# Kernel tuning notes

Measured on AMD Instinct MI355X. Metric: run time of the kernel, lower is better.

Reference implementation:

```python
import jax, jax.numpy as jnp
import numpy as np

VEC_DIM = 128   # D (also the per-head dim in this module)
HEADS = 8
PATCH = 4
WIN = 7
N_BATCH = 4
H_IMG = 448
W_IMG = 448


def _relative_index():
    # Swin-style relative position index, computed statically (matches torch code
    # which uses torch.meshgrid with default 'ij' indexing).
    coords = np.stack(np.meshgrid(np.arange(WIN), np.arange(WIN), indexing='ij'))  # [2,W,W]
    flat = coords.reshape(2, -1)                      # [2, W*W]
    rel = flat[:, :, None] - flat[:, None, :]         # [2, p, p]
    rel = rel.transpose(1, 2, 0).astype(np.int64)     # [p, p, 2]
    rel[:, :, 0] += WIN - 1
    rel[:, :, 1] += WIN - 1
    rel[:, :, 1] *= 2 * WIN - 1
    return rel.sum(-1)                                # [p, p], values in [0, (2W-1)^2)

REL_IDX = jnp.asarray(_relative_index())


def setup_inputs() -> dict:
    key = jax.random.key(0)
    ks = jax.random.split(key, 8)
    P = (H_IMG // PATCH) * (W_IMG // PATCH)  # 12544
    D, H = VEC_DIM, HEADS
    s = 0.02
    return {
        'x': jax.random.normal(ks[0], (N_BATCH, D, P), jnp.float32),
        'Wq': jax.random.normal(ks[1], (H * D, D), jnp.float32) * s,
        'bq': jnp.zeros((H * D,), jnp.float32),
        'Wk': jax.random.normal(ks[2], (H * D, D), jnp.float32) * s,
        'bk': jnp.zeros((H * D,), jnp.float32),
        'Wv': jax.random.normal(ks[3], (H * D, D), jnp.float32) * s,
        'bv': jnp.zeros((H * D,), jnp.float32),
        'Wo': jax.random.normal(ks[4], (D, H * D), jnp.float32) * s,
        'bo': jnp.zeros((D,), jnp.float32),
        'pos_code': jax.random.normal(ks[5], ((2 * WIN - 1) ** 2, H), jnp.float32) * s,
        'h': H_IMG,
        'w': W_IMG,
    }


def reference(x, Wq, bq, Wk, bk, Wv, bv, Wo, bo, pos_code, h, w):
    N, D, P = x.shape
    H = HEADS
    ch, cw = h // PATCH, w // PATCH
    nh, nw = ch // WIN, cw // WIN            # windows per axis
    p = WIN * WIN                            # tokens per window

    def emb(W, b):
        # pointwise Conv1d: [N,D,P] -> [N,H*D,P] -> [N,H,D,P]
        return (jnp.einsum('od,ndp->nop', W, x) + b[None, :, None]).reshape(N, H, D, P)

    def partition(e):
        # [N,H,D,P] -> [N,H,win_num,D,p]
        e = e.reshape(N, H, D, nh, WIN, nw, WIN)
        return e.transpose(0, 1, 3, 5, 2, 4, 6).reshape(N, H, nh * nw, D, p)

    q = partition(emb(Wq, bq))
    k = partition(emb(Wk, bk))
    v = partition(emb(Wv, bv))

    # attn[n,h,w,i,j] = sum_d k[n,h,w,d,i] * q[n,h,w,d,j], scaled
    attn = jnp.einsum('nhwdi,nhwdj->nhwij', k, q) / (D ** 0.5)
    bias = pos_code[REL_IDX].transpose(2, 0, 1)          # [H, p, p]
    attn = attn + bias[None, :, None, :, :]
    weights = jax.nn.softmax(attn, axis=3)               # softmax over key index i

    # out[n,h,w,d,j] = sum_i v[n,h,w,d,i] * weights[n,h,w,i,j]
    out = jnp.einsum('nhwdi,nhwij->nhwdj', v, weights)

    # window merge: [N,H,win_num,D,p] -> [N,H*D,P]
    out = out.reshape(N, H, nh, nw, D, WIN, WIN)
    out = out.transpose(0, 1, 4, 2, 5, 3, 6).reshape(N, H * D, P)

    return jnp.einsum('od,ndp->nop', Wo, out) + bo[None, :, None]
```

## Files before the change

kernel.cpp:

```cpp
#include <hip/hip_runtime.h>
#include <hip/hip_bf16.h>

typedef unsigned short u16;
typedef unsigned int u32;
typedef __attribute__((ext_vector_type(8))) short bf16x8;
typedef __attribute__((ext_vector_type(4))) float f32x4;
typedef __attribute__((ext_vector_type(2))) unsigned int u32x2;

#define NBATCH 4
#define DDIM   128
#define NHEAD  8
#define PTOT   12544
#define CWID   112
#define NTOK   49
#define PSTR   68
#define SCALE  0.08838834764831845f

#define BUFSZ   14464
#undef BUFSZ
#define BUFSZ   16384
#define OFF_US  8192
#define OFF_PL  32768
#define OFF_PCF 36100
#define OFF_MF  38804
#define OFF_CS  40852
#define LDS_TOT 41876

#undef OFF_MF
#undef OFF_CS
#undef LDS_TOT
#define OFF_CS  38804
#define LDS_TOT 39828

__device__ __forceinline__ float bf2f(u16 u) {
    union { u32 i; float f; } x; x.i = ((u32)u) << 16; return x.f;
}
__device__ __forceinline__ u16 f2bf(float f) {
    union { float f; u32 u; } v; v.f = f;
    return (u16)((v.u + 0x7fffu + ((v.u >> 16) & 1u)) >> 16);
}
__device__ __forceinline__ u32 pk2(float a, float b) {
    union { __hip_bfloat162 h; u32 u; } c;
    float2 t; t.x = a; t.y = b;
    c.h = __float22bfloat162_rn(t);
    return c.u;
}
__device__ __forceinline__ int swz128(int row, int col) {
    return row * 128 + ((((col >> 3) ^ (row & 15)) & 15) << 3) + (col & 7);
}

#define WS_WC   131072
#define WS_F32  262144

__global__ void __launch_bounds__(256) prep(
    const float* __restrict__ Wq, const float* __restrict__ Wk,
    const float* __restrict__ Wv, const float* __restrict__ Wo,
    const float* __restrict__ bq, const float* __restrict__ bk,
    const float* __restrict__ bv, u16* __restrict__ ws)
{
    __shared__ u16 lm[32768];
    const int tid = threadIdx.x;
    const int b = blockIdx.x;
    const bool isG = (b >= 8);
    const int h = b & 7;
    float* fb = (float*)(ws + WS_F32);

    if (!isG) {
        for (int idx = tid; idx < 16384; idx += 256) {
            const int dd = idx >> 7, dh = idx & 127;
            lm[swz128(dd, dh)] = f2bf(Wo[dd * 1024 + h * 128 + dh]);
        }
        for (int idx = tid; idx < 16384; idx += 256) {
            const int dh = idx >> 7, d = idx & 127;
            lm[16384 + swz128(d, dh)] = f2bf(Wv[(h * 128 + dh) * 128 + d]);
        }
        if (tid < 128) {
            float s = 0.f;
            for (int dh = 0; dh < 128; ++dh)
                s += Wo[tid * 1024 + h * 128 + dh] * bv[h * 128 + dh];
            fb[h * 128 + tid] = s;
        }
    } else {
        for (int idx = tid; idx < 16384; idx += 256) {
            const int dh = idx >> 7, d = idx & 127;
            lm[swz128(d, dh)] = f2bf(Wk[(h * 128 + dh) * 128 + d]);
        }
        for (int idx = tid; idx < 16384; idx += 256) {
            const int dh = idx >> 7, dp = idx & 127;
            lm[16384 + swz128(dp, dh)] = f2bf(Wq[(h * 128 + dh) * 128 + dp]);
        }
        if (tid < 128) {
            float r = 0.f, m = 0.f;
            for (int dh = 0; dh < 128; ++dh) {
                r += bk[h * 128 + dh] * Wq[(h * 128 + dh) * 128 + tid];
                m += Wk[(h * 128 + dh) * 128 + tid] * bq[h * 128 + dh];
            }
            fb[1024 + h * 128 + tid] = r * SCALE;
            fb[2048 + h * 128 + tid] = m * SCALE;
        }
        if (tid == 0) {
            float s = 0.f;
            for (int dh = 0; dh < 128; ++dh) s += bk[h * 128 + dh] * bq[h * 128 + dh];
            fb[3072 + h] = s * SCALE;
        }
    }
    __syncthreads();

    const int w = tid >> 6, lane = tid & 63, quad = lane >> 4, lid = lane & 15;
    const f32x4 z4 = {0.f, 0.f, 0.f, 0.f};
    u16* dst = ws + (isG ? 0 : WS_WC) + h * 16384;
    const float gs = isG ? SCALE : 1.0f;
    #pragma unroll
    for (int mtl = 0; mtl < 2; ++mtl) {
        const int mt = 2 * w + mtl;
        bf16x8 A[4];
        #pragma unroll
        for (int kt = 0; kt < 4; ++kt)
            A[kt] = *(const bf16x8*)(lm + swz128(mt * 16 + lid, kt * 32 + quad * 8));
        #pragma unroll
        for (int nt = 0; nt < 8; ++nt) {
            f32x4 acc = z4;
            #pragma unroll
            for (int kt = 0; kt < 4; ++kt) {
                bf16x8 B = *(const bf16x8*)(lm + 16384 + swz128(nt * 16 + lid, kt * 32 + quad * 8));
                acc = __builtin_amdgcn_mfma_f32_16x16x32_bf16(A[kt], B, acc, 0, 0, 0);
            }
            #pragma unroll
            for (int r = 0; r < 4; ++r) {
                const int row = mt * 16 + quad * 4 + r, col = nt * 16 + lid;
                if (isG) dst[col * 128 + row] = f2bf(acc[r] * gs);
                else     dst[row * 128 + col] = f2bf(acc[r]);
            }
        }
    }
}

__global__ void __launch_bounds__(256, 2)
winattn(const float* __restrict__ xg, const u16* __restrict__ ws,
        const float* __restrict__ bo, const float* __restrict__ posf,
        float* __restrict__ out)
{
    __shared__ __align__(16) u16 sm[LDS_TOT];
    u16* xw  = sm;
    u16* pl  = sm + OFF_PL;
    float* pcf = (float*)(sm + OFF_PCF);
    float* cs  = (float*)(sm + OFF_CS);

    const int tid  = threadIdx.x;
    const int w    = tid >> 6;
    const int lane = tid & 63;
    const int quad = lane >> 4;
    const int lid  = lane & 15;
    const int bx   = blockIdx.x;
    const int n    = bx >> 8;
    const int win  = bx & 255;
    const int pbase = (win >> 4) * 7 * CWID + (win & 15) * 7;

    const bf16x8 zf = {0,0,0,0,0,0,0,0};
    const f32x4  z4 = {0.f,0.f,0.f,0.f};

    const u16* Gt  = ws;
    const u16* Wcw = ws + WS_WC;
    const float* fb  = (const float*)(ws + WS_F32);
    const float* bcv = fb;
    const float* rP  = fb + 1024;
    const float* MP  = fb + 2048;
    const float* sP  = fb + 3072;

    for (int i = tid; i < 169 * NHEAD; i += 256) pcf[i] = posf[i];
    const float* xn = xg + n * DDIM * PTOT;
    for (int idx = tid; idx < DDIM * NTOK; idx += 256) {
        int d = idx / NTOK;
        int t = idx - d * NTOK;
        int a = t / 7, b = t - a * 7;
        xw[swz128(t, d)] = f2bf(xn[d * PTOT + pbase + a * CWID + b]);
    }
    __syncthreads();

    bf16x8 xfrag[4][4];
    #pragma unroll
    for (int mt = 0; mt < 4; ++mt)
        #pragma unroll
        for (int kt = 0; kt < 4; ++kt)
            xfrag[mt][kt] = (mt * 16 + lid < NTOK)
                ? *(const bf16x8*)(xw + swz128(mt * 16 + lid, kt * 32 + quad * 8)) : zf;
    const int j = 16 * w + lid;
    bf16x8 xq[4];
    #pragma unroll
    for (int kt = 0; kt < 4; ++kt)
        xq[kt] = (j < NTOK)
            ? *(const bf16x8*)(xw + swz128(j, kt * 32 + quad * 8)) : zf;

    for (int hh = w; hh < NHEAD; hh += 4) {
        const float sh = sP[hh];
        #pragma unroll
        for (int mt = 0; mt < 4; ++mt) {
            float c = 0.f;
            #pragma unroll
            for (int kt = 0; kt < 4; ++kt)
                #pragma unroll
                for (int jj = 0; jj < 8; ++jj)
                    c += bf2f((u16)xfrag[mt][kt][jj]) * MP[hh * 128 + kt * 32 + quad * 8 + jj];
            c += __shfl_xor(c, 16);
            c += __shfl_xor(c, 32);
            if (quad == 0) cs[hh * 64 + mt * 16 + lid] = c + sh;
        }
    }
    __syncthreads();

    f32x4 outacc[8];
    #pragma unroll
    for (int nt = 0; nt < 8; ++nt) outacc[nt] = z4;

    const int jc = j < NTOK ? j : NTOK - 1;

    for (int h = 0; h < NHEAD; ++h) {
        u16* tsb = sm + (h & 1) * BUFSZ;
        u16* usb = tsb + OFF_US;

        #pragma unroll
        for (int mtl = 0; mtl < 2; ++mtl) {
            const int mt = 2 * w + mtl;
            bf16x8 A[4];
            #pragma unroll
            for (int kt = 0; kt < 4; ++kt)
                A[kt] = *(const bf16x8*)(Gt + h * 16384 + (mt * 16 + lid) * 128 + kt * 32 + quad * 8);
            const f32x4 rb = *(const f32x4*)(rP + h * 128 + mt * 16 + quad * 4);
            const int dpb = mt * 16 + quad * 4;
            #pragma unroll
            for (int nt = 0; nt < 4; ++nt) {
                f32x4 acc = z4;
                #pragma unroll
                for (int kt = 0; kt < 4; ++kt)
                    acc = __builtin_amdgcn_mfma_f32_16x16x32_bf16(A[kt], xfrag[nt][kt], acc, 0, 0, 0);
                const int i = nt * 16 + lid;
                u32x2 pkv;
                pkv.x = pk2(acc[0] + rb[0], acc[1] + rb[1]);
                pkv.y = pk2(acc[2] + rb[2], acc[3] + rb[3]);
                *(u32x2*)(tsb + i * 128 + ((((dpb >> 3) ^ (i & 15)) & 15) << 3) + (dpb & 7)) = pkv;
            }
        }
        #pragma unroll
        for (int ntl = 0; ntl < 2; ++ntl) {
            const int nt = 2 * w + ntl;
            bf16x8 B[4];
            #pragma unroll
            for (int kt = 0; kt < 4; ++kt)
                B[kt] = *(const bf16x8*)(Wcw + h * 16384 + (nt * 16 + lid) * 128 + kt * 32 + quad * 8);
            const int dd = nt * 16 + lid;
            const float bb = bcv[h * 128 + dd];
            #pragma unroll
            for (int mt = 0; mt < 4; ++mt) {
                f32x4 acc = z4;
                #pragma unroll
                for (int kt = 0; kt < 4; ++kt)
                    acc = __builtin_amdgcn_mfma_f32_16x16x32_bf16(xfrag[mt][kt], B[kt], acc, 0, 0, 0);
                const int ib = mt * 16 + quad * 4;
                u32x2 pkv;
                pkv.x = pk2(acc[0] + bb, acc[1] + bb);
                pkv.y = pk2(acc[2] + bb, acc[3] + bb);
                *(u32x2*)(usb + dd * 64 + ((((ib >> 3) ^ (dd & 7)) & 7) << 3) + (ib & 7)) = pkv;
            }
        }
        __syncthreads();

        f32x4 S[4];
        #pragma unroll
        for (int mt = 0; mt < 4; ++mt) {
            S[mt] = z4;
            #pragma unroll
            for (int kt = 0; kt < 4; ++kt) {
                bf16x8 A = *(const bf16x8*)(tsb + (mt * 16 + lid) * 128 + ((((kt * 4 + quad) ^ lid) & 15) << 3));
                S[mt] = __builtin_amdgcn_mfma_f32_16x16x32_bf16(A, xq[kt], S[mt], 0, 0, 0);
            }
        }
        const int aj = jc / 7, bj = jc - aj * 7;
        float sv[4][4];
        float mx = -3.0e38f;
        #pragma unroll
        for (int mt = 0; mt < 4; ++mt)
            #pragma unroll
            for (int r = 0; r < 4; ++r) {
                const int ii = mt * 16 + quad * 4 + r;
                float vvv;
                if (ii < NTOK) {
                    const int ai = ii / 7, bi = ii - ai * 7;
                    const int rel = (ai - aj + 6) + 13 * (bi - bj + 6);
                    vvv = S[mt][r] + cs[h * 64 + ii] + pcf[rel * NHEAD + h];
                } else {
                    vvv = -3.0e38f;
                }
                sv[mt][r] = vvv;
                mx = fmaxf(mx, vvv);
            }
        mx = fmaxf(mx, __shfl_xor(mx, 16));
        mx = fmaxf(mx, __shfl_xor(mx, 32));
        float ssum = 0.f;
        #pragma unroll
        for (int mt = 0; mt < 4; ++mt)
            #pragma unroll
            for (int r = 0; r < 4; ++r) {
                const float e = __expf(sv[mt][r] - mx);
                sv[mt][r] = e;
                ssum += e;
            }
        ssum += __shfl_xor(ssum, 16);
        ssum += __shfl_xor(ssum, 32);
        const float inv = 1.0f / ssum;
        if (j < NTOK) {
            #pragma unroll
            for (int mt = 0; mt < 4; ++mt) {
                u32x2 pkv;
                pkv.x = pk2(sv[mt][0] * inv, sv[mt][1] * inv);
                pkv.y = pk2(sv[mt][2] * inv, sv[mt][3] * inv);
                *(u32x2*)(pl + j * PSTR + mt * 16 + quad * 4) = pkv;
            }
        }
        __threadfence_block();

        #pragma unroll
        for (int kt = 0; kt < 2; ++kt) {
            union { bf16x8 v; u32 u[4]; } Af;
            #pragma unroll
            for (int q2 = 0; q2 < 4; ++q2)
                Af.u[q2] = *(const u32*)(pl + jc * PSTR + kt * 32 + quad * 8 + 2 * q2);
            #pragma unroll
            for (int nt = 0; nt < 8; ++nt) {
                const int dd = nt * 16 + lid;
                bf16x8 Bu = *(const bf16x8*)(usb + dd * 64 + ((((kt * 4 + quad) ^ (dd & 7)) & 7) << 3));
                outacc[nt] = __builtin_amdgcn_mfma_f32_16x16x32_bf16(Af.v, Bu, outacc[nt], 0, 0, 0);
            }
        }
    }

    float* outp = out + n * DDIM * PTOT;
    #pragma unroll
    for (int nt = 0; nt < 8; ++nt) {
        const int dd = nt * 16 + lid;
        const float bov = bo[dd];
        #pragma unroll
        for (int r = 0; r < 4; ++r) {
            const int jj = 16 * w + quad * 4 + r;
            if (jj < NTOK) {
                const int a = jj / 7, b = jj - a * 7;
                outp[dd * PTOT + pbase + a * CWID + b] = outacc[nt][r] + bov;
            }
        }
    }
}

extern "C" void kernel_launch(void* const* d_in, const int* in_sizes, int n_in,
                              void* d_out, int out_size, void* d_ws, size_t ws_size,
                              hipStream_t stream) {
    (void)in_sizes; (void)n_in; (void)ws_size; (void)out_size;
    prep<<<16, 256, 0, stream>>>((const float*)d_in[1], (const float*)d_in[3],
                                 (const float*)d_in[5], (const float*)d_in[7],
                                 (const float*)d_in[2], (const float*)d_in[4],
                                 (const float*)d_in[6], (u16*)d_ws);
    winattn<<<NBATCH * 256, 256, 0, stream>>>(
        (const float*)d_in[0], (const u16*)d_ws,
        (const float*)d_in[8], (const float*)d_in[9], (float*)d_out);
}
```

Before: 236.6 us.

## Shrink LDS to single buffer, raise occupancy, and split prep across more blocks

The per-head T/U buffers are no longer double-buffered, and the positional-bias table is stored as bf16 in LDS. Together these cut shared memory roughly in half, so launch bounds rise to allow 4 blocks per CU. A __syncthreads at the end of each head iteration replaces the double-buffer hazard protection, and T stores are skipped for padding rows. The prep kernel is split into 128 blocks, each computing 16 output rows, to use more CUs; the trade-off is an extra barrier per head, possible register spills under the tighter bound, and slightly reduced bias precision.

```diff
diff --git a/kernel.cpp b/kernel.cpp
--- a/kernel.cpp
+++ b/kernel.cpp
@@ -16,21 +16,11 @@
 #define PSTR   68
 #define SCALE  0.08838834764831845f
 
-#define BUFSZ   14464
-#undef BUFSZ
-#define BUFSZ   16384
-#define OFF_US  8192
-#define OFF_PL  32768
-#define OFF_PCF 36100
-#define OFF_MF  38804
-#define OFF_CS  40852
-#define LDS_TOT 41876
-
-#undef OFF_MF
-#undef OFF_CS
-#undef LDS_TOT
-#define OFF_CS  38804
-#define LDS_TOT 39828
+#define OFF_US  6272
+#define OFF_PL  14464
+#define OFF_PCF 17796
+#define OFF_CS  19148
+#define LDS_TOT 20172
 
 __device__ __forceinline__ float bf2f(u16 u) {
     union { u32 i; float f; } x; x.i = ((u32)u) << 16; return x.f;
@@ -58,38 +48,41 @@
     const float* __restrict__ bq, const float* __restrict__ bk,
     const float* __restrict__ bv, u16* __restrict__ ws)
 {
-    __shared__ u16 lm[32768];
+    __shared__ u16 lm[18432];
     const int tid = threadIdx.x;
-    const int b = blockIdx.x;
+    const int bb  = blockIdx.x;
+    const int b   = bb >> 3;
+    const int sub = bb & 7;
     const bool isG = (b >= 8);
     const int h = b & 7;
+    const int r0 = sub * 16;
     float* fb = (float*)(ws + WS_F32);
 
     if (!isG) {
-        for (int idx = tid; idx < 16384; idx += 256) {
-            const int dd = idx >> 7, dh = idx & 127;
-            lm[swz128(dd, dh)] = f2bf(Wo[dd * 1024 + h * 128 + dh]);
+        for (int idx = tid; idx < 2048; idx += 256) {
+            const int lr = idx >> 7, dh = idx & 127;
+            lm[swz128(lr, dh)] = f2bf(Wo[(r0 + lr) * 1024 + h * 128 + dh]);
         }
         for (int idx = tid; idx < 16384; idx += 256) {
             const int dh = idx >> 7, d = idx & 127;
-            lm[16384 + swz128(d, dh)] = f2bf(Wv[(h * 128 + dh) * 128 + d]);
-        }
-        if (tid < 128) {
+            lm[2048 + swz128(d, dh)] = f2bf(Wv[(h * 128 + dh) * 128 + d]);
+        }
+        if (sub == 0 && tid < 128) {
             float s = 0.f;
             for (int dh = 0; dh < 128; ++dh)
                 s += Wo[tid * 1024 + h * 128 + dh] * bv[h * 128 + dh];
             fb[h * 128 + tid] = s;
         }
     } else {
-        for (int idx = tid; idx < 16384; idx += 256) {
-            const int dh = idx >> 7, d = idx & 127;
-            lm[swz128(d, dh)] = f2bf(Wk[(h * 128 + dh) * 128 + d]);
+        for (int idx = tid; idx < 2048; idx += 256) {
+            const int dh = idx >> 4, lr = idx & 15;
+            lm[swz128(lr, dh)] = f2bf(Wk[(h * 128 + dh) * 128 + r0 + lr]);
         }
         for (int idx = tid; idx < 16384; idx += 256) {
             const int dh = idx >> 7, dp = idx & 127;
-            lm[16384 + swz128(dp, dh)] = f2bf(Wq[(h * 128 + dh) * 128 + dp]);
-        }
-        if (tid < 128) {
+            lm[2048 + swz128(dp, dh)] = f2bf(Wq[(h * 128 + dh) * 128 + dp]);
+        }
+        if (sub == 0 && tid < 128) {
             float r = 0.f, m = 0.f;
             for (int dh = 0; dh < 128; ++dh) {
                 r += bk[h * 128 + dh] * Wq[(h * 128 + dh) * 128 + tid];
@@ -98,7 +91,7 @@
             fb[1024 + h * 128 + tid] = r * SCALE;
             fb[2048 + h * 128 + tid] = m * SCALE;
         }
-        if (tid == 0) {
+        if (sub == 0 && tid == 0) {
             float s = 0.f;
             for (int dh = 0; dh < 128; ++dh) s += bk[h * 128 + dh] * bq[h * 128 + dh];
             fb[3072 + h] = s * SCALE;
@@ -110,40 +103,37 @@
     const f32x4 z4 = {0.f, 0.f, 0.f, 0.f};
     u16* dst = ws + (isG ? 0 : WS_WC) + h * 16384;
     const float gs = isG ? SCALE : 1.0f;
-    #pragma unroll
-    for (int mtl = 0; mtl < 2; ++mtl) {
-        const int mt = 2 * w + mtl;
-        bf16x8 A[4];
-        #pragma unroll
-        for (int kt = 0; kt < 4; ++kt)
-            A[kt] = *(const bf16x8*)(lm + swz128(mt * 16 + lid, kt * 32 + quad * 8));
-        #pragma unroll
-        for (int nt = 0; nt < 8; ++nt) {
-            f32x4 acc = z4;
-            #pragma unroll
-            for (int kt = 0; kt < 4; ++kt) {
-                bf16x8 B = *(const bf16x8*)(lm + 16384 + swz128(nt * 16 + lid, kt * 32 + quad * 8));
-                acc = __builtin_amdgcn_mfma_f32_16x16x32_bf16(A[kt], B, acc, 0, 0, 0);
-            }
-            #pragma unroll
-            for (int r = 0; r < 4; ++r) {
-                const int row = mt * 16 + quad * 4 + r, col = nt * 16 + lid;
-                if (isG) dst[col * 128 + row] = f2bf(acc[r] * gs);
-                else     dst[row * 128 + col] = f2bf(acc[r]);
-            }
-        }
-    }
-}
-
-__global__ void __launch_bounds__(256, 2)
+    bf16x8 A[4];
+    #pragma unroll
+    for (int kt = 0; kt < 4; ++kt)
+        A[kt] = *(const bf16x8*)(lm + swz128(lid, kt * 32 + quad * 8));
+    #pragma unroll
+    for (int ntl = 0; ntl < 2; ++ntl) {
+        const int nt = 2 * w + ntl;
+        f32x4 acc = z4;
+        #pragma unroll
+        for (int kt = 0; kt < 4; ++kt) {
+            bf16x8 B = *(const bf16x8*)(lm + 2048 + swz128(nt * 16 + lid, kt * 32 + quad * 8));
+            acc = __builtin_amdgcn_mfma_f32_16x16x32_bf16(A[kt], B, acc, 0, 0, 0);
+        }
+        #pragma unroll
+        for (int r = 0; r < 4; ++r) {
+            const int row = r0 + quad * 4 + r, col = nt * 16 + lid;
+            if (isG) dst[col * 128 + row] = f2bf(acc[r] * gs);
+            else     dst[row * 128 + col] = f2bf(acc[r]);
+        }
+    }
+}
+
+__global__ void __launch_bounds__(256, 4)
 winattn(const float* __restrict__ xg, const u16* __restrict__ ws,
         const float* __restrict__ bo, const float* __restrict__ posf,
         float* __restrict__ out)
 {
     __shared__ __align__(16) u16 sm[LDS_TOT];
-    u16* xw  = sm;
-    u16* pl  = sm + OFF_PL;
-    float* pcf = (float*)(sm + OFF_PCF);
+    u16* xw    = sm;
+    u16* pl    = sm + OFF_PL;
+    u16* pcf16 = sm + OFF_PCF;
     float* cs  = (float*)(sm + OFF_CS);
 
     const int tid  = threadIdx.x;
@@ -167,7 +157,7 @@
     const float* MP  = fb + 2048;
     const float* sP  = fb + 3072;
 
-    for (int i = tid; i < 169 * NHEAD; i += 256) pcf[i] = posf[i];
+    for (int i = tid; i < 169 * NHEAD; i += 256) pcf16[i] = f2bf(posf[i]);
     const float* xn = xg + n * DDIM * PTOT;
     for (int idx = tid; idx < DDIM * NTOK; idx += 256) {
         int d = idx / NTOK;
@@ -214,10 +204,10 @@
 
     const int jc = j < NTOK ? j : NTOK - 1;
 
+    u16* tsb = sm;
+    u16* usb = sm + OFF_US;
+
     for (int h = 0; h < NHEAD; ++h) {
-        u16* tsb = sm + (h & 1) * BUFSZ;
-        u16* usb = tsb + OFF_US;
-
         #pragma unroll
         for (int mtl = 0; mtl < 2; ++mtl) {
             const int mt = 2 * w + mtl;
@@ -234,10 +224,12 @@
                 for (int kt = 0; kt < 4; ++kt)
                     acc = __builtin_amdgcn_mfma_f32_16x16x32_bf16(A[kt], xfrag[nt][kt], acc, 0, 0, 0);
                 const int i = nt * 16 + lid;
-                u32x2 pkv;
-                pkv.x = pk2(acc[0] + rb[0], acc[1] + rb[1]);
-                pkv.y = pk2(acc[2] + rb[2], acc[3] + rb[3]);
-                *(u32x2*)(tsb + i * 128 + ((((dpb >> 3) ^ (i & 15)) & 15) << 3) + (dpb & 7)) = pkv;
+                if (i < NTOK) {
+                    u32x2 pkv;
+                    pkv.x = pk2(acc[0] + rb[0], acc[1] + rb[1]);
+                    pkv.y = pk2(acc[2] + rb[2], acc[3] + rb[3]);
+                    *(u32x2*)(tsb + i * 128 + ((((dpb >> 3) ^ (i & 15)) & 15) << 3) + (dpb & 7)) = pkv;
+                }
             }
         }
         #pragma unroll
@@ -286,7 +278,7 @@
                 if (ii < NTOK) {
                     const int ai = ii / 7, bi = ii - ai * 7;
                     const int rel = (ai - aj + 6) + 13 * (bi - bj + 6);
-                    vvv = S[mt][r] + cs[h * 64 + ii] + pcf[rel * NHEAD + h];
+                    vvv = S[mt][r] + cs[h * 64 + ii] + bf2f(pcf16[rel * NHEAD + h]);
                 } else {
                     vvv = -3.0e38f;
                 }
@@ -331,6 +323,7 @@
                 outacc[nt] = __builtin_amdgcn_mfma_f32_16x16x32_bf16(Af.v, Bu, outacc[nt], 0, 0, 0);
             }
         }
+        if (h < NHEAD - 1) __syncthreads();
     }
 
     float* outp = out + n * DDIM * PTOT;
@@ -353,10 +346,10 @@
                               void* d_out, int out_size, void* d_ws, size_t ws_size,
                               hipStream_t stream) {
     (void)in_sizes; (void)n_in; (void)ws_size; (void)out_size;
-    prep<<<16, 256, 0, stream>>>((const float*)d_in[1], (const float*)d_in[3],
-                                 (const float*)d_in[5], (const float*)d_in[7],
-                                 (const float*)d_in[2], (const float*)d_in[4],
-                                 (const float*)d_in[6], (u16*)d_ws);
+    prep<<<128, 256, 0, stream>>>((const float*)d_in[1], (const float*)d_in[3],
+                                  (const float*)d_in[5], (const float*)d_in[7],
+                                  (const float*)d_in[2], (const float*)d_in[4],
+                                  (const float*)d_in[6], (u16*)d_ws);
     winattn<<<NBATCH * 256, 256, 0, stream>>>(
         (const float*)d_in[0], (const u16*)d_ws,
         (const float*)d_in[8], (const float*)d_in[9], (float*)d_out);
```

After: 342.7 us. +44.8%, slower.
